# Kernel optimization log

Hardware: AMD Instinct MI355X
Metric: run time of the kernel (lower is better)

## Reference

```python
import jax, jax.numpy as jnp
import numpy as np

B, N, DM, S = 128, 1024, 64, 2
D_IN = 1 + 1 + 2 + DM  # x(1) + m(1) + u(2) + h(DM)


def setup_inputs() -> dict:
    key = jax.random.key(0)
    ks = jax.random.split(key, 12)
    return {
        "x": jax.random.normal(ks[0], (B, 1, N), jnp.float32),
        "m": jax.random.uniform(ks[1], (B, 1, N), jnp.float32),
        "u": jax.random.normal(ks[2], (B, 2, N), jnp.float32),
        "h": jax.random.normal(ks[3], (B, DM, N), jnp.float32),
        # stack of support_len row-normalized-ish adjacencies [S, N, N]
        "adj": jax.random.uniform(ks[4], (S, N, N), jnp.float32) / N,
        "W_in": jax.random.normal(ks[5], (DM, D_IN), jnp.float32) * 0.05,
        "b_in": jnp.zeros((DM,), jnp.float32),
        "W_gc": jax.random.normal(ks[6], (DM, S * DM), jnp.float32) * 0.05,
        "b_gc": jnp.zeros((DM,), jnp.float32),
        "W_out": jax.random.normal(ks[7], (DM, 2 * DM), jnp.float32) * 0.05,
        "b_out": jnp.zeros((DM,), jnp.float32),
        "W_read": jax.random.normal(ks[8], (1, 2 * DM), jnp.float32) * 0.05,
        "b_read": jnp.zeros((1,), jnp.float32),
        "prelu_w": jnp.full((1,), 0.25, jnp.float32),
    }


def _conv1x1(x, W, b):
    # Conv1d(kernel_size=1): [b,c,n] x [o,c] -> [b,o,n]
    return jnp.einsum('bcn,oc->bon', x, W) + b[None, :, None]


def reference(x, m, u, h, adj, W_in, b_in, W_gc, b_gc, W_out, b_out, W_read, b_read, prelu_w):
    # concat inputs on channel dim, then 1x1 conv to d_model
    x_in = jnp.concatenate([x, m, u, h], axis=1)            # [b, d_in, n]
    x_in = _conv1x1(x_in, W_in, b_in)                        # [b, dm, n]
    # SpatialConvOrderK (order=1, include_self=False):
    # per-support aggregation einsum('ncvl,wv->ncwl') with l==1
    agg = jnp.einsum('bcv,swv->bscw', x_in, adj)             # [b, S, dm, n]
    b_, s_, c_, n_ = agg.shape
    agg = agg.reshape(b_, s_ * c_, n_)                       # support-major concat
    gc = _conv1x1(agg, W_gc, b_gc)                           # [b, dm, n]
    out = jnp.concatenate([gc, h], axis=1)                   # [b, 2dm, n]
    out = _conv1x1(out, W_out, b_out)
    out = jnp.where(out >= 0, out, prelu_w[0] * out)         # PReLU (1 param)
    out = jnp.concatenate([out, h], axis=1)                  # [b, 2dm, n]
    return _conv1x1(out, W_read, b_read), out
```

## Files before the change

kernel.cpp:

```cpp
#include <hip/hip_runtime.h>
#include <hip/hip_bf16.h>
#include <stdint.h>

#define NB 128
#define NN 1024
#define NDM 64

typedef __bf16 bf16;
typedef __bf16 bf16x8_t __attribute__((ext_vector_type(8)));
typedef __bf16 bf16x4_t __attribute__((ext_vector_type(4)));
typedef float f32x4 __attribute__((ext_vector_type(4)));

__global__ __launch_bounds__(256) void k_prep(
    const float* __restrict__ adj,
    const float* __restrict__ W_in, const float* __restrict__ b_in,
    const float* __restrict__ W_gc, const float* __restrict__ b_gc,
    const float* __restrict__ W_out, const float* __restrict__ b_out,
    const float* __restrict__ W_read,
    bf16* __restrict__ adjb, bf16* __restrict__ WAT, float* __restrict__ WYX,
    float* __restrict__ BIAS, bf16* __restrict__ W1B, bf16* __restrict__ A2B,
    float* __restrict__ HBv) {
  const int bx = blockIdx.x;
  if (bx < 2048) {
    int i = bx * 256 + threadIdx.x;
    float4 v = reinterpret_cast<const float4*>(adj)[i];
    bf16x4_t r;
    r.x = (bf16)v.x; r.y = (bf16)v.y; r.z = (bf16)v.z; r.w = (bf16)v.w;
    reinterpret_cast<bf16x4_t*>(adjb)[i] = r;
    return;
  }
  int i = (bx - 2048) * 256 + threadIdx.x;
  if (i < 8192) {
    int r = i >> 6, cc = i & 63;
    int cq = cc >> 3, j = cc & 7;
    int c = ((cq ^ (r & 7)) << 3) + j;
    int s = r >> 6, o = r & 63;
    float val = 0.f;
    for (int k = 0; k < 64; ++k) val += W_gc[o * 128 + s * 64 + k] * W_in[k * 68 + 4 + c];
    WAT[i] = (bf16)val;
  } else if (i < 8704) {
    int idx = i - 8192;
    int r = idx >> 2, jj = idx & 3;
    int s = r >> 6, o = r & 63;
    float val = 0.f;
    for (int k = 0; k < 64; ++k) val += W_gc[o * 128 + s * 64 + k] * W_in[k * 68 + jj];
    WYX[idx] = val;
  } else if (i < 8832) {
    int r = i - 8704;
    int s = r >> 6, o = r & 63;
    float val = 0.f;
    for (int k = 0; k < 64; ++k) val += W_gc[o * 128 + s * 64 + k] * b_in[k];
    BIAS[r] = val;
  } else if (i < 12928) {
    int j = i - 8832;
    int o = j >> 6, c = j & 63;
    W1B[j] = (bf16)W_out[o * 128 + c];
  } else if (i < 18048) {
    int j = i - 12928;
    int r = j >> 6, c = j & 63;
    float val = 0.f;
    if (r < 64) val = W_out[r * 128 + 64 + c];
    else if (r == 64) val = W_read[64 + c];
    A2B[j] = (bf16)val;
  } else if (i < 18112) {
    int o = i - 18048;
    float val = b_out[o];
    for (int c = 0; c < 64; ++c) val += W_out[o * 128 + c] * b_gc[c];
    HBv[o] = val;
  }
}

__global__ __launch_bounds__(256) void k_build(
    const float* __restrict__ x, const float* __restrict__ m, const float* __restrict__ u,
    const float* __restrict__ h, const bf16* __restrict__ WAT,
    const float* __restrict__ WYX, const float* __restrict__ BIAS,
    bf16* __restrict__ Y, bf16* __restrict__ HT, float* __restrict__ out2) {
  __shared__ __align__(16) float T[64 * 128];
  __shared__ __align__(16) bf16 HTs[128 * 64];
  __shared__ __align__(16) bf16 WAs[128 * 64];
  __shared__ __align__(16) float X4L[128 * 4];
  __shared__ __align__(16) float WYXs[128 * 4];
  __shared__ __align__(16) float biasL[128];
  const int t = threadIdx.x;
  const int vb = blockIdx.x * 128;
  const int b = blockIdx.y;

  for (int i = t; i < 2048; i += 256)
    __builtin_amdgcn_global_load_lds(
        (const uint32_t*)(h + (size_t)(b * 64 + (i >> 5)) * NN + vb + (i & 31) * 4),
        (uint32_t*)&T[i * 4], 16, 0, 0);
  for (int i = t; i < 1024; i += 256)
    __builtin_amdgcn_global_load_lds((const uint32_t*)(WAT + i * 8), (uint32_t*)&WAs[i * 8], 16, 0, 0);
  if (t < 128)
    __builtin_amdgcn_global_load_lds((const uint32_t*)(WYX + t * 4), (uint32_t*)&WYXs[t * 4], 16, 0, 0);
  if (t < 32)
    __builtin_amdgcn_global_load_lds((const uint32_t*)(BIAS + t * 4), (uint32_t*)&biasL[t * 4], 16, 0, 0);
  if (t < 128) {
    float4 x4;
    x4.x = x[(size_t)b * NN + vb + t];
    x4.y = m[(size_t)b * NN + vb + t];
    x4.z = u[(size_t)(b * 2) * NN + vb + t];
    x4.w = u[(size_t)(b * 2 + 1) * NN + vb + t];
    *reinterpret_cast<float4*>(&X4L[t * 4]) = x4;
  }
  __syncthreads();

  {
    const int v = t >> 1, half = t & 1;
#pragma unroll
    for (int cc = 0; cc < 4; ++cc) {
      int cq = half * 4 + cc;
      int cbase = (cq ^ (v & 7)) << 3;
      bf16x8_t pk;
#pragma unroll
      for (int j = 0; j < 8; ++j) pk[j] = (bf16)T[(cbase + j) * 128 + v];
      *reinterpret_cast<bf16x8_t*>(&HTs[v * 64 + cq * 8]) = pk;
      *reinterpret_cast<bf16x8_t*>(&HT[((size_t)(b << 10) + vb + v) * 64 + cq * 8]) = pk;
    }
  }
  for (int i = t; i < 2048; i += 256) {
    int r = i >> 5, ck = i & 31;
    float4 hv = *reinterpret_cast<const float4*>(&T[r * 128 + ck * 4]);
    *reinterpret_cast<float4*>(&out2[(size_t)(b * 128 + 64 + r) * NN + vb + ck * 4]) = hv;
  }
  __syncthreads();

  const int wave = t >> 6, lane = t & 63;
  const int q = lane >> 4, lx = lane & 7, o16 = lane & 15;
  const int offK0 = (q ^ lx) << 3, offK1 = ((q + 4) ^ lx) << 3;

#pragma unroll
  for (int vi = 0; vi < 2; ++vi) {
    const int vt = wave + vi * 4;
    const int vrow = vt * 16 + o16;
    bf16x8_t af0 = *reinterpret_cast<const bf16x8_t*>(&HTs[vrow * 64 + offK0]);
    bf16x8_t af1 = *reinterpret_cast<const bf16x8_t*>(&HTs[vrow * 64 + offK1]);
    float4 x4r[4];
#pragma unroll
    for (int r = 0; r < 4; ++r)
      x4r[r] = *reinterpret_cast<const float4*>(&X4L[(vt * 16 + q * 4 + r) * 4]);
    const int vg = vb + vt * 16 + q * 4;
    for (int nt = 0; nt < 8; ++nt) {
      const int rr = nt * 16 + o16;
      bf16x8_t bf0 = *reinterpret_cast<const bf16x8_t*>(&WAs[rr * 64 + offK0]);
      bf16x8_t bf1 = *reinterpret_cast<const bf16x8_t*>(&WAs[rr * 64 + offK1]);
      float bsv = biasL[rr];
      float4 wy = *reinterpret_cast<const float4*>(&WYXs[rr * 4]);
      f32x4 c0;
#pragma unroll
      for (int r = 0; r < 4; ++r)
        c0[r] = bsv + wy.x * x4r[r].x + wy.y * x4r[r].y + wy.z * x4r[r].z + wy.w * x4r[r].w;
      f32x4 acc = __builtin_amdgcn_mfma_f32_16x16x32_bf16(af0, bf0, c0, 0, 0, 0);
      acc = __builtin_amdgcn_mfma_f32_16x16x32_bf16(af1, bf1, acc, 0, 0, 0);
      const int s = nt >> 2;
      const int o = rr - s * 64;
      bf16x4_t pk;
      pk.x = (bf16)acc[0]; pk.y = (bf16)acc[1]; pk.z = (bf16)acc[2]; pk.w = (bf16)acc[3];
      *reinterpret_cast<bf16x4_t*>(&Y[(size_t)(b * 64 + o) * 2048 + s * 1024 + vg]) = pk;
    }
  }
}

__global__ __launch_bounds__(256) void k_gemm(
    const bf16* __restrict__ Y, const bf16* __restrict__ ADJB,
    const bf16* __restrict__ HT,
    const bf16* __restrict__ W1B, const bf16* __restrict__ A2B,
    const float* __restrict__ HBv, const float* __restrict__ W_read,
    const float* __restrict__ b_read, const float* __restrict__ prelu_w,
    float* __restrict__ out0, float* __restrict__ out2) {
  __shared__ __align__(16) union SMem {
    struct { bf16 As[128 * 64]; bf16 Bs[128 * 64]; } st;
    bf16 gcs[2 * 128 * 72];
  } sm;
  __shared__ __align__(16) bf16 W1s[64 * 72];
  __shared__ __align__(16) bf16 A2s[80 * 72];
  __shared__ float HBs[64];
  __shared__ float Wrs[64];

  const int t = threadIdx.x;
  const int wave = t >> 6, lane = t & 63;
  const int rowA = blockIdx.x * 128;
  const int colB = blockIdx.y * 128;
  const int wm = (wave & 1) * 64, wn = (wave >> 1) * 64;
  const int fr = lane & 15;
  const int q = lane >> 4, lx = lane & 7;
  const int offK0 = (q ^ lx) << 3, offK1 = ((q + 4) ^ lx) << 3;

  for (int i = t; i < 4096; i += 256) W1s[(i >> 6) * 72 + (i & 63)] = W1B[i];
  for (int i = t; i < 5120; i += 256) A2s[(i >> 6) * 72 + (i & 63)] = A2B[i];
  if (t < 64) { HBs[t] = HBv[t]; Wrs[t] = W_read[t]; }
  const float pw = prelu_w[0];
  const float br = b_read[0];

  f32x4 acc[4][4];
  const f32x4 zero = {0.f, 0.f, 0.f, 0.f};
#pragma unroll
  for (int i = 0; i < 4; ++i)
#pragma unroll
    for (int j = 0; j < 4; ++j) acc[i][j] = zero;

  const bf16* aSrc[4]; const bf16* bSrc[4];
  uint32_t* aDst[4]; uint32_t* bDst[4];
#pragma unroll
  for (int j = 0; j < 4; ++j) {
    int c = t + 256 * j;
    int row = c >> 3;
    int qs = (c & 7) ^ (row & 7);
    aSrc[j] = Y + (size_t)(rowA + row) * 2048 + qs * 8;
    bSrc[j] = ADJB + (size_t)(colB + row) * 1024 + qs * 8;
    aDst[j] = (uint32_t*)&sm.st.As[c * 8];
    bDst[j] = (uint32_t*)&sm.st.Bs[c * 8];
  }
  int rAb[4], rBb[4];
#pragma unroll
  for (int i = 0; i < 4; ++i) {
    rAb[i] = (wm + i * 16 + fr) * 64;
    rBb[i] = (wn + i * 16 + fr) * 64;
  }
  __syncthreads();

  for (int s = 0; s < 2; ++s) {
    for (int kk = 0; kk < 1024; kk += 64) {
#pragma unroll
      for (int j = 0; j < 4; ++j) {
        __builtin_amdgcn_global_load_lds((const uint32_t*)aSrc[j], aDst[j], 16, 0, 0);
        aSrc[j] += 64;
      }
#pragma unroll
      for (int j = 0; j < 4; ++j) {
        __builtin_amdgcn_global_load_lds((const uint32_t*)bSrc[j], bDst[j], 16, 0, 0);
        bSrc[j] += 64;
      }
      __syncthreads();
#pragma unroll
      for (int k2 = 0; k2 < 2; ++k2) {
        const int off = k2 ? offK1 : offK0;
        bf16x8_t af[4], bfr[4];
#pragma unroll
        for (int i = 0; i < 4; ++i)
          af[i] = *reinterpret_cast<const bf16x8_t*>(&sm.st.As[rAb[i] + off]);
#pragma unroll
        for (int i = 0; i < 4; ++i)
          bfr[i] = *reinterpret_cast<const bf16x8_t*>(&sm.st.Bs[rBb[i] + off]);
#pragma unroll
        for (int i = 0; i < 4; ++i)
#pragma unroll
          for (int j = 0; j < 4; ++j)
            acc[i][j] = __builtin_amdgcn_mfma_f32_16x16x32_bf16(af[i], bfr[j], acc[i][j], 0, 0, 0);
      }
      __syncthreads();
    }
    if (s == 0) {
#pragma unroll
      for (int j = 0; j < 4; ++j) bSrc[j] += (1024 * 1024 - 1024);
    }
  }

  {
    const int b2w = wm >> 6;
#pragma unroll
    for (int i = 0; i < 4; ++i) {
      const int cc0 = i * 16 + q * 4;
#pragma unroll
      for (int j = 0; j < 4; ++j) {
        const int wl = wn + j * 16 + fr;
        bf16x4_t r;
        r.x = (bf16)acc[i][j][0]; r.y = (bf16)acc[i][j][1];
        r.z = (bf16)acc[i][j][2]; r.w = (bf16)acc[i][j][3];
        *reinterpret_cast<bf16x4_t*>(&sm.gcs[b2w * 9216 + wl * 72 + cc0]) = r;
      }
    }
  }
  __syncthreads();

  const int b2 = wave >> 1, jh = wave & 1;
  const int b = blockIdx.x * 2 + b2;

  f32x4 acc2[5][4];
#pragma unroll
  for (int i = 0; i < 5; ++i)
#pragma unroll
    for (int j = 0; j < 4; ++j) {
      if (i < 4) {
        f32x4 c0;
#pragma unroll
        for (int r = 0; r < 4; ++r) c0[r] = HBs[i * 16 + q * 4 + r];
        acc2[i][j] = c0;
      } else {
        acc2[i][j] = zero;
      }
    }

#pragma unroll
  for (int k2 = 0; k2 < 64; k2 += 32) {
    bf16x8_t af2[4], bf2[4];
#pragma unroll
    for (int i = 0; i < 4; ++i)
      af2[i] = *reinterpret_cast<const bf16x8_t*>(&W1s[(i * 16 + fr) * 72 + k2 + q * 8]);
#pragma unroll
    for (int j = 0; j < 4; ++j)
      bf2[j] = *reinterpret_cast<const bf16x8_t*>(&sm.gcs[b2 * 9216 + (jh * 64 + j * 16 + fr) * 72 + k2 + q * 8]);
#pragma unroll
    for (int i = 0; i < 4; ++i)
#pragma unroll
      for (int j = 0; j < 4; ++j)
        acc2[i][j] = __builtin_amdgcn_mfma_f32_16x16x32_bf16(af2[i], bf2[j], acc2[i][j], 0, 0, 0);
  }

#pragma unroll
  for (int k2 = 0; k2 < 64; k2 += 32) {
    const int off = k2 ? offK1 : offK0;
    bf16x8_t bh[4], af3[5];
#pragma unroll
    for (int j = 0; j < 4; ++j) {
      const int w = colB + jh * 64 + j * 16 + fr;
      bh[j] = *reinterpret_cast<const bf16x8_t*>(&HT[((size_t)(b << 10) + w) * 64 + off]);
    }
#pragma unroll
    for (int i = 0; i < 5; ++i)
      af3[i] = *reinterpret_cast<const bf16x8_t*>(&A2s[(i * 16 + fr) * 72 + k2 + q * 8]);
#pragma unroll
    for (int i = 0; i < 5; ++i)
#pragma unroll
      for (int j = 0; j < 4; ++j)
        acc2[i][j] = __builtin_amdgcn_mfma_f32_16x16x32_bf16(af3[i], bh[j], acc2[i][j], 0, 0, 0);
  }

  float rd[4] = {0.f, 0.f, 0.f, 0.f};
#pragma unroll
  for (int i = 0; i < 4; ++i) {
#pragma unroll
    for (int r = 0; r < 4; ++r) {
      const int o = i * 16 + q * 4 + r;
      const float wr = Wrs[o];
#pragma unroll
      for (int j = 0; j < 4; ++j) {
        const int wg = colB + jh * 64 + j * 16 + fr;
        float val = acc2[i][j][r];
        val = val >= 0.f ? val : pw * val;
        out2[(size_t)(b * 128 + o) * 1024 + wg] = val;
        rd[j] += wr * val;
      }
    }
  }
#pragma unroll
  for (int j = 0; j < 4; ++j) {
    rd[j] += __shfl_xor(rd[j], 16, 64);
    rd[j] += __shfl_xor(rd[j], 32, 64);
  }
  if (lane < 16) {
#pragma unroll
    for (int j = 0; j < 4; ++j) {
      const int wg = colB + jh * 64 + j * 16 + lane;
      out0[(size_t)b * 1024 + wg] = rd[j] + acc2[4][j][0] + br;
    }
  }
}

extern "C" void kernel_launch(void* const* d_in, const int* in_sizes, int n_in,
                              void* d_out, int out_size, void* d_ws, size_t ws_size,
                              hipStream_t stream) {
  (void)in_sizes; (void)n_in; (void)out_size; (void)ws_size;
  const float* x       = (const float*)d_in[0];
  const float* m       = (const float*)d_in[1];
  const float* u       = (const float*)d_in[2];
  const float* h       = (const float*)d_in[3];
  const float* adj     = (const float*)d_in[4];
  const float* W_in    = (const float*)d_in[5];
  const float* b_in    = (const float*)d_in[6];
  const float* W_gc    = (const float*)d_in[7];
  const float* b_gc    = (const float*)d_in[8];
  const float* W_out   = (const float*)d_in[9];
  const float* b_out   = (const float*)d_in[10];
  const float* W_read  = (const float*)d_in[11];
  const float* b_read  = (const float*)d_in[12];
  const float* prelu_w = (const float*)d_in[13];

  char* ws = (char*)d_ws;
  bf16*  Y    = (bf16*)(ws);
  bf16*  ADJB = (bf16*)(ws + 33554432);
  bf16*  HT   = (bf16*)(ws + 37748736);
  bf16*  WAT  = (bf16*)(ws + 54525952);
  float* WYX  = (float*)(ws + 54542336);
  float* BIAS = (float*)(ws + 54544384);
  bf16*  W1B  = (bf16*)(ws + 54544896);
  bf16*  A2B  = (bf16*)(ws + 54553088);
  float* HBv  = (float*)(ws + 54563328);

  float* out0 = (float*)d_out;
  float* out2 = out0 + 131072;

  hipLaunchKernelGGL(k_prep,  dim3(2119),     dim3(256), 0, stream,
                     adj, W_in, b_in, W_gc, b_gc, W_out, b_out, W_read,
                     ADJB, WAT, WYX, BIAS, W1B, A2B, HBv);
  hipLaunchKernelGGL(k_build, dim3(8, 128),   dim3(256), 0, stream,
                     x, m, u, h, WAT, WYX, BIAS, Y, HT, out2);
  hipLaunchKernelGGL(k_gemm,  dim3(64, 8),    dim3(256), 0, stream,
                     Y, ADJB, HT, W1B, A2B, HBv, W_read, b_read, prelu_w, out0, out2);
}
```

Baseline: 183.1 us.

## Double-buffer adjacency GEMM with 256-row tiles, 8 waves and XCD-aware block mapping

Restructures the main GEMM so each block covers 256 rows of Y with 512 threads. It double-buffers the LDS stages and issues the next tile's async global-to-LDS loads between the two MFMA half-steps, using explicit waitcnt, barriers and setprio. The linear block index is remapped so blocks on the same XCD share A rows, improving L2 reuse, and the weight loads into LDS are vectorised. The goal is to hide global load latency and cut the synchronisation bubbles of the single-buffered loop. The cost is larger LDS use and manual vmcnt accounting that must match the number of loads issued per stage.

```diff
diff --git a/kernel.cpp b/kernel.cpp
--- a/kernel.cpp
+++ b/kernel.cpp
@@ -161,7 +161,7 @@
   }
 }
 
-__global__ __launch_bounds__(256) void k_gemm(
+__global__ __launch_bounds__(512, 2) void k_gemm(
     const bf16* __restrict__ Y, const bf16* __restrict__ ADJB,
     const bf16* __restrict__ HT,
     const bf16* __restrict__ W1B, const bf16* __restrict__ A2B,
@@ -169,8 +169,8 @@
     const float* __restrict__ b_read, const float* __restrict__ prelu_w,
     float* __restrict__ out0, float* __restrict__ out2) {
   __shared__ __align__(16) union SMem {
-    struct { bf16 As[128 * 64]; bf16 Bs[128 * 64]; } st;
-    bf16 gcs[2 * 128 * 72];
+    struct { bf16 As[2][256 * 64]; bf16 Bs[2][128 * 64]; } st;
+    bf16 gcs[4 * 128 * 72];
   } sm;
   __shared__ __align__(16) bf16 W1s[64 * 72];
   __shared__ __align__(16) bf16 A2s[80 * 72];
@@ -179,15 +179,25 @@
 
   const int t = threadIdx.x;
   const int wave = t >> 6, lane = t & 63;
-  const int rowA = blockIdx.x * 128;
-  const int colB = blockIdx.y * 128;
-  const int wm = (wave & 1) * 64, wn = (wave >> 1) * 64;
+  const int lin = blockIdx.y * 32 + blockIdx.x;
+  const int xcd = lin & 7, rest = lin >> 3;
+  const int rowA = (xcd * 4 + (rest >> 3)) * 256;
+  const int colB = (rest & 7) * 128;
+  const int wm = (wave >> 1) * 64, wn = (wave & 1) * 64;
   const int fr = lane & 15;
   const int q = lane >> 4, lx = lane & 7;
   const int offK0 = (q ^ lx) << 3, offK1 = ((q + 4) ^ lx) << 3;
 
-  for (int i = t; i < 4096; i += 256) W1s[(i >> 6) * 72 + (i & 63)] = W1B[i];
-  for (int i = t; i < 5120; i += 256) A2s[(i >> 6) * 72 + (i & 63)] = A2B[i];
+  {
+    const int r = t >> 3, c8 = t & 7;
+    *reinterpret_cast<bf16x8_t*>(&W1s[r * 72 + c8 * 8]) =
+        *reinterpret_cast<const bf16x8_t*>(&W1B[t * 8]);
+  }
+  for (int i = t; i < 640; i += 512) {
+    const int r = i >> 3, c8 = i & 7;
+    *reinterpret_cast<bf16x8_t*>(&A2s[r * 72 + c8 * 8]) =
+        *reinterpret_cast<const bf16x8_t*>(&A2B[i * 8]);
+  }
   if (t < 64) { HBs[t] = HBv[t]; Wrs[t] = W_read[t]; }
   const float pw = prelu_w[0];
   const float br = b_read[0];
@@ -199,61 +209,76 @@
 #pragma unroll
     for (int j = 0; j < 4; ++j) acc[i][j] = zero;
 
-  const bf16* aSrc[4]; const bf16* bSrc[4];
-  uint32_t* aDst[4]; uint32_t* bDst[4];
-#pragma unroll
-  for (int j = 0; j < 4; ++j) {
-    int c = t + 256 * j;
-    int row = c >> 3;
-    int qs = (c & 7) ^ (row & 7);
-    aSrc[j] = Y + (size_t)(rowA + row) * 2048 + qs * 8;
-    bSrc[j] = ADJB + (size_t)(colB + row) * 1024 + qs * 8;
-    aDst[j] = (uint32_t*)&sm.st.As[c * 8];
-    bDst[j] = (uint32_t*)&sm.st.Bs[c * 8];
-  }
+  auto stage = [&](int d, int kt) {
+    const int kg = kt * 64;
+    const int s = kg >> 10, v0 = kg & 1023;
+#pragma unroll
+    for (int ja = 0; ja < 4; ++ja) {
+      const int c = t + 512 * ja;
+      const int row = c >> 3;
+      const int qs = ((c & 7) ^ (row & 7)) << 3;
+      __builtin_amdgcn_global_load_lds(
+          (const uint32_t*)(Y + (size_t)(rowA + row) * 2048 + kg + qs),
+          (uint32_t*)&sm.st.As[d][c * 8], 16, 0, 0);
+    }
+#pragma unroll
+    for (int jb = 0; jb < 2; ++jb) {
+      const int c = t + 512 * jb;
+      const int row = c >> 3;
+      const int qs = ((c & 7) ^ (row & 7)) << 3;
+      __builtin_amdgcn_global_load_lds(
+          (const uint32_t*)(ADJB + ((size_t)s << 20) + (size_t)(colB + row) * 1024 + v0 + qs),
+          (uint32_t*)&sm.st.Bs[d][c * 8], 16, 0, 0);
+    }
+  };
+
   int rAb[4], rBb[4];
 #pragma unroll
   for (int i = 0; i < 4; ++i) {
     rAb[i] = (wm + i * 16 + fr) * 64;
     rBb[i] = (wn + i * 16 + fr) * 64;
   }
-  __syncthreads();
-
-  for (int s = 0; s < 2; ++s) {
-    for (int kk = 0; kk < 1024; kk += 64) {
-#pragma unroll
-      for (int j = 0; j < 4; ++j) {
-        __builtin_amdgcn_global_load_lds((const uint32_t*)aSrc[j], aDst[j], 16, 0, 0);
-        aSrc[j] += 64;
-      }
-#pragma unroll
-      for (int j = 0; j < 4; ++j) {
-        __builtin_amdgcn_global_load_lds((const uint32_t*)bSrc[j], bDst[j], 16, 0, 0);
-        bSrc[j] += 64;
-      }
-      __syncthreads();
-#pragma unroll
-      for (int k2 = 0; k2 < 2; ++k2) {
-        const int off = k2 ? offK1 : offK0;
-        bf16x8_t af[4], bfr[4];
-#pragma unroll
-        for (int i = 0; i < 4; ++i)
-          af[i] = *reinterpret_cast<const bf16x8_t*>(&sm.st.As[rAb[i] + off]);
-#pragma unroll
-        for (int i = 0; i < 4; ++i)
-          bfr[i] = *reinterpret_cast<const bf16x8_t*>(&sm.st.Bs[rBb[i] + off]);
-#pragma unroll
-        for (int i = 0; i < 4; ++i)
-#pragma unroll
-          for (int j = 0; j < 4; ++j)
-            acc[i][j] = __builtin_amdgcn_mfma_f32_16x16x32_bf16(af[i], bfr[j], acc[i][j], 0, 0, 0);
-      }
-      __syncthreads();
-    }
-    if (s == 0) {
-#pragma unroll
-      for (int j = 0; j < 4; ++j) bSrc[j] += (1024 * 1024 - 1024);
-    }
+
+  stage(0, 0);
+  stage(1, 1);
+
+#pragma unroll 2
+  for (int kt = 0; kt < 32; ++kt) {
+    const int cur = kt & 1;
+    if (kt < 31) asm volatile("s_waitcnt vmcnt(6)" ::: "memory");
+    else         asm volatile("s_waitcnt vmcnt(0)" ::: "memory");
+    __builtin_amdgcn_s_barrier();
+    const bf16* A_ = sm.st.As[cur];
+    const bf16* B_ = sm.st.Bs[cur];
+    bf16x8_t af0[4], bf0[4], af1[4], bf1[4];
+#pragma unroll
+    for (int i = 0; i < 4; ++i) af0[i] = *reinterpret_cast<const bf16x8_t*>(&A_[rAb[i] + offK0]);
+#pragma unroll
+    for (int i = 0; i < 4; ++i) bf0[i] = *reinterpret_cast<const bf16x8_t*>(&B_[rBb[i] + offK0]);
+    asm volatile("s_waitcnt lgkmcnt(0)" ::: "memory");
+    __builtin_amdgcn_sched_barrier(0);
+    __builtin_amdgcn_s_setprio(1);
+#pragma unroll
+    for (int i = 0; i < 4; ++i)
+#pragma unroll
+      for (int j = 0; j < 4; ++j)
+        acc[i][j] = __builtin_amdgcn_mfma_f32_16x16x32_bf16(af0[i], bf0[j], acc[i][j], 0, 0, 0);
+    __builtin_amdgcn_s_setprio(0);
+#pragma unroll
+    for (int i = 0; i < 4; ++i) af1[i] = *reinterpret_cast<const bf16x8_t*>(&A_[rAb[i] + offK1]);
+#pragma unroll
+    for (int i = 0; i < 4; ++i) bf1[i] = *reinterpret_cast<const bf16x8_t*>(&B_[rBb[i] + offK1]);
+    asm volatile("s_waitcnt lgkmcnt(0)" ::: "memory");
+    __builtin_amdgcn_sched_barrier(0);
+    __builtin_amdgcn_s_barrier();
+    if (kt < 30) stage(cur, kt + 2);
+    __builtin_amdgcn_s_setprio(1);
+#pragma unroll
+    for (int i = 0; i < 4; ++i)
+#pragma unroll
+      for (int j = 0; j < 4; ++j)
+        acc[i][j] = __builtin_amdgcn_mfma_f32_16x16x32_bf16(af1[i], bf1[j], acc[i][j], 0, 0, 0);
+    __builtin_amdgcn_s_setprio(0);
   }
 
   {
@@ -274,7 +299,7 @@
   __syncthreads();
 
   const int b2 = wave >> 1, jh = wave & 1;
-  const int b = blockIdx.x * 2 + b2;
+  const int b = (rowA >> 6) + b2;
 
   f32x4 acc2[5][4];
 #pragma unroll
@@ -395,6 +420,6 @@
                      ADJB, WAT, WYX, BIAS, W1B, A2B, HBv);
   hipLaunchKernelGGL(k_build, dim3(8, 128),   dim3(256), 0, stream,
                      x, m, u, h, WAT, WYX, BIAS, Y, HT, out2);
-  hipLaunchKernelGGL(k_gemm,  dim3(64, 8),    dim3(256), 0, stream,
+  hipLaunchKernelGGL(k_gemm,  dim3(32, 8),    dim3(512), 0, stream,
                      Y, ADJB, HT, W1B, A2B, HBv, W_read, b_read, prelu_w, out0, out2);
 }
```

After: 182.6 us. About the same (-0.3%).
